# Performance work log

Measured on AMD Instinct MI355X. Metric: run time of the kernel, lower is better.

The kernel has to match this reference:

```python
import jax, jax.numpy as jnp
import numpy as np

B, T, F = 4096, 64, 32
U1, U2 = 256, 128  # stacked GRU: rnn_units, rnn_units // 2


def _gru_layer(x, Wg, bg, Wc, bc, units):
    """TF GRUCell semantics over a full sequence.
    x: [B, T, D]. Wg: [D+U, 2U], Wc: [D+U, U]. Returns outputs [B, T, U].
    r,u = sigmoid([x,h] Wg + bg); c = tanh([x, r*h] Wc + bc); h' = u*h + (1-u)*c
    """
    xT = jnp.swapaxes(x, 0, 1)  # [T, B, D]
    h0 = jnp.zeros((x.shape[0], units), x.dtype)

    def step(h, xt):
        gates = jax.nn.sigmoid(jnp.concatenate([xt, h], axis=-1) @ Wg + bg)
        r, u = jnp.split(gates, 2, axis=-1)
        c = jnp.tanh(jnp.concatenate([xt, r * h], axis=-1) @ Wc + bc)
        h_new = u * h + (1.0 - u) * c
        return h_new, h_new

    _, outs = jax.lax.scan(step, h0, xT)
    return jnp.swapaxes(outs, 0, 1)  # [B, T, U]


def setup_inputs() -> dict:
    key = jax.random.key(0)
    ks = jax.random.split(key, 12)
    s = 0.1
    inp = {
        "frames": jax.random.normal(ks[0], (B, T, F), jnp.float32),
        "W1_g": jax.random.normal(ks[1], (F + U1, 2 * U1), jnp.float32) * s,
        "b1_g": jnp.ones((2 * U1,), jnp.float32),  # TF gate bias init = 1.0
        "W1_c": jax.random.normal(ks[2], (F + U1, U1), jnp.float32) * s,
        "b1_c": jnp.zeros((U1,), jnp.float32),
        "W2_g": jax.random.normal(ks[3], (U1 + U2, 2 * U2), jnp.float32) * s,
        "b2_g": jnp.ones((2 * U2,), jnp.float32),
        "W2_c": jax.random.normal(ks[4], (U1 + U2, U2), jnp.float32) * s,
        "b2_c": jnp.zeros((U2,), jnp.float32),
        "Wd": jax.random.normal(ks[5], (U2, F), jnp.float32) * s,
        "bd": jnp.zeros((F,), jnp.float32),
    }
    return inp


def reference(frames, W1_g, b1_g, W1_c, b1_c, W2_g, b2_g, W2_c, b2_c, Wd, bd):
    # stacked GRU: MultiRNNCell([GRUCell(U1), GRUCell(U1 // 2)])
    h1 = _gru_layer(frames, W1_g, b1_g, W1_c, b1_c, U1)   # [B, T, U1]
    h2 = _gru_layer(h1, W2_g, b2_g, W2_c, b2_c, U2)       # [B, T, U2]
    last = h2[:, -1]                                       # use_cell_state=False -> outputs[:, -1]
    predicted = last @ Wd + bd                             # dense to sensor_count
    return predicted
```

## Files before the change

kernel.cpp:

```cpp
#include <hip/hip_runtime.h>


typedef unsigned short u16;
typedef __attribute__((ext_vector_type(8))) short bhalf8;
typedef __attribute__((ext_vector_type(4))) float fx4;

constexpr int Bc = 4096, Tc = 64, Fc = 32, U1 = 256, U2 = 128;
constexpr int K1 = Fc + U1;
constexpr int K2 = U1 + U2;
constexpr int NB = 16, NTHR = 512;
constexpr int LD1 = K1 + 8;
constexpr int LD2 = K2 + 8;

constexpr int nW1g = K1 * 512, nW1c = K1 * 256, nW2g = K2 * 256, nW2c = K2 * 128;
constexpr int oW1g = 0;
constexpr int oW1c = oW1g + nW1g;
constexpr int oW2g = oW1c + nW1c;
constexpr int oW2c = oW2g + nW2g;
constexpr int WTOT = oW2c + nW2c;
constexpr int nWdT = Fc * U2;

#define LGKM_BARRIER() asm volatile("s_waitcnt lgkmcnt(0)\n\ts_barrier" ::: "memory")

__device__ __forceinline__ u16 bf16_rne(float x) {
  unsigned u = __float_as_uint(x);
  return (u16)((u + 0x7fffu + ((u >> 16) & 1u)) >> 16);
}
__device__ __forceinline__ float bf16_f(u16 h) {
  return __uint_as_float(((unsigned)h) << 16);
}
__device__ __forceinline__ float sigm(float x) { return 1.0f / (1.0f + __expf(-x)); }
__device__ __forceinline__ float tanh_(float x) {
  x = fminf(fmaxf(x, -15.0f), 15.0f);
  const float s = __expf(2.0f * x);
  return (s - 1.0f) / (s + 1.0f);
}

__global__ void prep_weights(const float* __restrict__ W1g, const float* __restrict__ W1c,
                             const float* __restrict__ W2g, const float* __restrict__ W2c,
                             const float* __restrict__ Wd, u16* __restrict__ ws) {
  int j = blockIdx.x * 256 + threadIdx.x;
  if (j >= WTOT + nWdT) return;
  if (j >= WTOT) {
    const int jj = j - WTOT;
    float* wdT = (float*)(ws + WTOT);
    const int o = jj >> 7, c = jj & 127;
    wdT[jj] = Wd[c * Fc + o];
    return;
  }
  const float* src; u16* dst; int K, N, jj;
  if (j < nW1g)                    { src = W1g; K = K1; N = 512; jj = j;                      dst = ws + oW1g; }
  else if (j < nW1g + nW1c)        { src = W1c; K = K1; N = 256; jj = j - nW1g;               dst = ws + oW1c; }
  else if (j < nW1g + nW1c + nW2g) { src = W2g; K = K2; N = 256; jj = j - nW1g - nW1c;        dst = ws + oW2g; }
  else                             { src = W2c; K = K2; N = 128; jj = j - nW1g - nW1c - nW2g; dst = ws + oW2c; }
  int n = jj / K, k = jj - n * K;
  dst[(size_t)n * K + k] = bf16_rne(src[(size_t)k * N + n]);
}

template <int NT, int D>
struct Pipe {
  const u16* wp[NT];
  bhalf8 bb[D][NT];
  __device__ __forceinline__ void init(const u16* __restrict__ W, const int* n0,
                                       int K, int lc, int ao) {
#pragma unroll
    for (int i = 0; i < NT; ++i) wp[i] = W + (size_t)(n0[i] + lc) * K + ao;
  }
  __device__ __forceinline__ void prefetch() {
#pragma unroll
    for (int d = 0; d < D; ++d)
#pragma unroll
      for (int i = 0; i < NT; ++i) bb[d][i] = *(const bhalf8*)(wp[i] + d * 32);
  }
  template <int KT, int LDA>
  __device__ __forceinline__ void mm(fx4 (&acc)[NT], const u16 (&Ah)[16][LDA],
                                     const u16 (&Al)[16][LDA], int lc, int ao) {
#pragma unroll
    for (int kt = 0; kt < KT; ++kt) {
      const int k0 = kt * 32;
      const bhalf8 a_h = *(const bhalf8*)&Ah[lc][k0 + ao];
      const bhalf8 a_l = *(const bhalf8*)&Al[lc][k0 + ao];
#pragma unroll
      for (int i = 0; i < NT; ++i) {
        acc[i] = __builtin_amdgcn_mfma_f32_16x16x32_bf16(a_h, bb[kt % D][i], acc[i], 0, 0, 0);
        acc[i] = __builtin_amdgcn_mfma_f32_16x16x32_bf16(a_l, bb[kt % D][i], acc[i], 0, 0, 0);
      }
      if (kt + D < KT) {
#pragma unroll
        for (int i = 0; i < NT; ++i) bb[kt % D][i] = *(const bhalf8*)(wp[i] + (kt + D) * 32);
      }
    }
  }
};

__global__ __launch_bounds__(NTHR, 2)
void gru_mfma(const float* __restrict__ frames, const u16* __restrict__ ws,
              const float* __restrict__ b1g, const float* __restrict__ b1c,
              const float* __restrict__ b2g, const float* __restrict__ b2c,
              const float* __restrict__ bd, float* __restrict__ out) {
  __shared__ alignas(16) u16 A1h[16][LD1], A1l[16][LD1];
  __shared__ alignas(16) u16 A2h[16][LD2], A2l[16][LD2];

  const int tid = threadIdx.x;
  const int w = tid >> 6;
  const int l = tid & 63;
  const int lc = l & 15;
  const int lk = l >> 4;
  const int ao = lk * 8;
  const int row0 = lk * 4;
  const int b0 = blockIdx.x * NB;

  const float bg1r0 = b1g[w * 32 + lc],       bg1r1 = b1g[w * 32 + 16 + lc];
  const float bg1u0 = b1g[256 + w * 32 + lc], bg1u1 = b1g[256 + w * 32 + 16 + lc];
  const float bc10  = b1c[w * 32 + lc],       bc11  = b1c[w * 32 + 16 + lc];
  const float bg2r  = b2g[w * 16 + lc],       bg2u  = b2g[128 + w * 16 + lc];
  const float bc2v  = b2c[w * 16 + lc];

  Pipe<4, 4> pG1;  Pipe<2, 4> pC1;  Pipe<2, 4> pG2;  Pipe<1, 4> pC2;
  const int n0g1[4] = {w * 32, w * 32 + 16, 256 + w * 32, 256 + w * 32 + 16};
  const int n0c1[2] = {w * 32, w * 32 + 16};
  const int n0g2[2] = {w * 16, 128 + w * 16};
  const int n0c2[1] = {w * 16};
  pG1.init(ws + oW1g, n0g1, K1, lc, ao);
  pC1.init(ws + oW1c, n0c1, K1, lc, ao);
  pG2.init(ws + oW2g, n0g2, K2, lc, ao);
  pC2.init(ws + oW2c, n0c2, K2, lc, ao);

  for (int i = tid; i < 16 * LD1; i += NTHR) { (&A1h[0][0])[i] = 0; (&A1l[0][0])[i] = 0; }
  for (int i = tid; i < 16 * LD2; i += NTHR) { (&A2h[0][0])[i] = 0; (&A2l[0][0])[i] = 0; }

  const int xb = tid >> 5, xf = tid & 31;
  const float* fptr = frames + (size_t)(b0 + xb) * (Tc * Fc) + xf;

  {
    const float x0 = fptr[0];
    const u16 h = bf16_rne(x0);
    A1h[xb][xf] = h;
    A1l[xb][xf] = bf16_rne(x0 - bf16_f(h));
  }
  pG1.prefetch();
  LGKM_BARRIER();

  for (int t = 0; t < Tc; ++t) {
    const float xnxt = (t + 1 < Tc) ? fptr[(t + 1) * Fc] : 0.0f;

    fx4 acc[4] = { {bg1r0, bg1r0, bg1r0, bg1r0}, {bg1r1, bg1r1, bg1r1, bg1r1},
                   {bg1u0, bg1u0, bg1u0, bg1u0}, {bg1u1, bg1u1, bg1u1, bg1u1} };
    pG1.mm<9, LD1>(acc, A1h, A1l, lc, ao);
    pC1.prefetch();

    float hold1[2][4];
#pragma unroll
    for (int i = 0; i < 2; ++i)
#pragma unroll
      for (int q = 0; q < 4; ++q) {
        const int row = row0 + q, col = w * 32 + i * 16 + lc;
        hold1[i][q] = bf16_f(A1h[row][Fc + col]) + bf16_f(A1l[row][Fc + col]);
      }
    float rr[2][4], uu[2][4];
#pragma unroll
    for (int i = 0; i < 2; ++i)
#pragma unroll
      for (int q = 0; q < 4; ++q) { rr[i][q] = sigm(acc[i][q]); uu[i][q] = sigm(acc[2 + i][q]); }
    LGKM_BARRIER();

#pragma unroll
    for (int i = 0; i < 2; ++i)
#pragma unroll
      for (int q = 0; q < 4; ++q) {
        const int row = row0 + q, col = w * 32 + i * 16 + lc;
        const float rh = rr[i][q] * hold1[i][q];
        const u16 hh = bf16_rne(rh);
        A1h[row][Fc + col] = hh;
        A1l[row][Fc + col] = bf16_rne(rh - bf16_f(hh));
      }
    LGKM_BARRIER();

    fx4 accc[2] = { {bc10, bc10, bc10, bc10}, {bc11, bc11, bc11, bc11} };
    pC1.mm<9, LD1>(accc, A1h, A1l, lc, ao);
    pG2.prefetch();

    float hn1[2][4]; u16 hh1[2][4], hl1[2][4];
#pragma unroll
    for (int i = 0; i < 2; ++i)
#pragma unroll
      for (int q = 0; q < 4; ++q) {
        const float c = tanh_(accc[i][q]);
        const float hn = c + uu[i][q] * (hold1[i][q] - c);
        hh1[i][q] = bf16_rne(hn);
        hl1[i][q] = bf16_rne(hn - bf16_f(hh1[i][q]));
      }
    LGKM_BARRIER();
#pragma unroll
    for (int i = 0; i < 2; ++i)
#pragma unroll
      for (int q = 0; q < 4; ++q) {
        const int row = row0 + q, col = w * 32 + i * 16 + lc;
        A1h[row][Fc + col] = hh1[i][q];  A1l[row][Fc + col] = hl1[i][q];
        A2h[row][col] = hh1[i][q];       A2l[row][col] = hl1[i][q];
      }
    LGKM_BARRIER();

    fx4 acc2[2] = { {bg2r, bg2r, bg2r, bg2r}, {bg2u, bg2u, bg2u, bg2u} };
    pG2.mm<12, LD2>(acc2, A2h, A2l, lc, ao);
    pC2.prefetch();

    float hold2[4];
#pragma unroll
    for (int q = 0; q < 4; ++q) {
      const int row = row0 + q, col = w * 16 + lc;
      hold2[q] = bf16_f(A2h[row][U1 + col]) + bf16_f(A2l[row][U1 + col]);
    }
    float rr2[4], uu2[4];
#pragma unroll
    for (int q = 0; q < 4; ++q) { rr2[q] = sigm(acc2[0][q]); uu2[q] = sigm(acc2[1][q]); }
    LGKM_BARRIER();

#pragma unroll
    for (int q = 0; q < 4; ++q) {
      const int row = row0 + q, col = w * 16 + lc;
      const float rh = rr2[q] * hold2[q];
      const u16 hh = bf16_rne(rh);
      A2h[row][U1 + col] = hh;
      A2l[row][U1 + col] = bf16_rne(rh - bf16_f(hh));
    }
    LGKM_BARRIER();

    fx4 acc3[1] = { {bc2v, bc2v, bc2v, bc2v} };
    pC2.mm<12, LD2>(acc3, A2h, A2l, lc, ao);
    pG1.prefetch();
    LGKM_BARRIER();

#pragma unroll
    for (int q = 0; q < 4; ++q) {
      const int row = row0 + q, col = w * 16 + lc;
      const float c = tanh_(acc3[0][q]);
      const float hn = c + uu2[q] * (hold2[q] - c);
      const u16 hh = bf16_rne(hn);
      A2h[row][U1 + col] = hh;
      A2l[row][U1 + col] = bf16_rne(hn - bf16_f(hh));
    }
    {
      const u16 h = bf16_rne(xnxt);
      A1h[xb][xf] = h;
      A1l[xb][xf] = bf16_rne(xnxt - bf16_f(h));
    }
    LGKM_BARRIER();
  }

  {
    const float* wdT = (const float*)(ws + WTOT);
    const int o = tid & 31, b = tid >> 5;
    const float4* wrow = (const float4*)(wdT + o * 128);
    float acc = bd[o];
#pragma unroll 8
    for (int c4 = 0; c4 < 32; ++c4) {
      const float4 wv = wrow[c4];
      const int c = c4 * 4;
      const float h0 = bf16_f(A2h[b][U1 + c + 0]) + bf16_f(A2l[b][U1 + c + 0]);
      const float h1 = bf16_f(A2h[b][U1 + c + 1]) + bf16_f(A2l[b][U1 + c + 1]);
      const float h2 = bf16_f(A2h[b][U1 + c + 2]) + bf16_f(A2l[b][U1 + c + 2]);
      const float h3 = bf16_f(A2h[b][U1 + c + 3]) + bf16_f(A2l[b][U1 + c + 3]);
      acc = fmaf(h0, wv.x, fmaf(h1, wv.y, fmaf(h2, wv.z, fmaf(h3, wv.w, acc))));
    }
    out[(size_t)(b0 + b) * Fc + o] = acc;
  }
}

extern "C" void kernel_launch(void* const* d_in, const int* in_sizes, int n_in,
                              void* d_out, int out_size, void* d_ws, size_t ws_size,
                              hipStream_t stream) {
  const float* frames = (const float*)d_in[0];
  const float* W1g = (const float*)d_in[1];
  const float* b1g = (const float*)d_in[2];
  const float* W1c = (const float*)d_in[3];
  const float* b1c = (const float*)d_in[4];
  const float* W2g = (const float*)d_in[5];
  const float* b2g = (const float*)d_in[6];
  const float* W2c = (const float*)d_in[7];
  const float* b2c = (const float*)d_in[8];
  const float* Wd  = (const float*)d_in[9];
  const float* bd  = (const float*)d_in[10];
  u16* ws = (u16*)d_ws;
  float* outp = (float*)d_out;

  hipLaunchKernelGGL(prep_weights, dim3((WTOT + nWdT + 255) / 256), dim3(256), 0, stream,
                     W1g, W1c, W2g, W2c, Wd, ws);
  hipLaunchKernelGGL(gru_mfma, dim3(Bc / NB), dim3(NTHR), 0, stream,
                     frames, ws, b1g, b1c, b2g, b2c, bd, outp);
}
```

Measured before the change: 881.1 us.

## Write r*h into separate LDS buffers to drop per-step barriers

Stores r*h for both GRU layers in dedicated shared-memory buffers instead of overwriting the hidden state in place. This lets the kernel remove several block-wide barriers per timestep (from 7 to 4), since h_old no longer has to be protected before it is overwritten. It also merges the h_new compute and store loops and deepens the weight prefetch pipelines for three of the four matmuls (depth 4 raised to 6 or 8). The costs are more shared memory, now allocated dynamically, and more registers held by the deeper prefetch buffers, which could hurt occupancy at two blocks per CU.

```diff
diff --git a/kernel.cpp b/kernel.cpp
--- a/kernel.cpp
+++ b/kernel.cpp
@@ -2,6 +2,7 @@
 
 
 typedef unsigned short u16;
+typedef unsigned int u32;
 typedef __attribute__((ext_vector_type(8))) short bhalf8;
 typedef __attribute__((ext_vector_type(4))) float fx4;
 
@@ -9,8 +10,10 @@
 constexpr int K1 = Fc + U1;
 constexpr int K2 = U1 + U2;
 constexpr int NB = 16, NTHR = 512;
-constexpr int LD1 = K1 + 8;
-constexpr int LD2 = K2 + 8;
+constexpr int LD1 = 296;
+constexpr int LD2 = 392;
+constexpr int LDR1 = 264;
+constexpr int LDR2 = 136;
 
 constexpr int nW1g = K1 * 512, nW1c = K1 * 256, nW2g = K2 * 256, nW2c = K2 * 128;
 constexpr int oW1g = 0;
@@ -19,6 +22,17 @@
 constexpr int oW2c = oW2g + nW2g;
 constexpr int WTOT = oW2c + nW2c;
 constexpr int nWdT = Fc * U2;
+
+constexpr int oA1h = 0;
+constexpr int oA1l = oA1h + 16 * LD1;
+constexpr int oA2h = oA1l + 16 * LD1;
+constexpr int oA2l = oA2h + 16 * LD2;
+constexpr int oR1h = oA2l + 16 * LD2;
+constexpr int oR1l = oR1h + 16 * LDR1;
+constexpr int oR2h = oR1l + 16 * LDR1;
+constexpr int oR2l = oR2h + 16 * LDR2;
+constexpr int SM_TOT = oR2l + 16 * LDR2;
+constexpr size_t SMEM_BYTES = (size_t)SM_TOT * 2;
 
 #define LGKM_BARRIER() asm volatile("s_waitcnt lgkmcnt(0)\n\ts_barrier" ::: "memory")
 
@@ -57,7 +71,7 @@
   dst[(size_t)n * K + k] = bf16_rne(src[(size_t)k * N + n]);
 }
 
-template <int NT, int D>
+template <int NT, int D, int KT>
 struct Pipe {
   const u16* wp[NT];
   bhalf8 bb[D][NT];
@@ -72,34 +86,35 @@
 #pragma unroll
       for (int i = 0; i < NT; ++i) bb[d][i] = *(const bhalf8*)(wp[i] + d * 32);
   }
-  template <int KT, int LDA>
-  __device__ __forceinline__ void mm(fx4 (&acc)[NT], const u16 (&Ah)[16][LDA],
-                                     const u16 (&Al)[16][LDA], int lc, int ao) {
-#pragma unroll
-    for (int kt = 0; kt < KT; ++kt) {
-      const int k0 = kt * 32;
-      const bhalf8 a_h = *(const bhalf8*)&Ah[lc][k0 + ao];
-      const bhalf8 a_l = *(const bhalf8*)&Al[lc][k0 + ao];
-#pragma unroll
-      for (int i = 0; i < NT; ++i) {
-        acc[i] = __builtin_amdgcn_mfma_f32_16x16x32_bf16(a_h, bb[kt % D][i], acc[i], 0, 0, 0);
-        acc[i] = __builtin_amdgcn_mfma_f32_16x16x32_bf16(a_l, bb[kt % D][i], acc[i], 0, 0, 0);
-      }
-      if (kt + D < KT) {
-#pragma unroll
-        for (int i = 0; i < NT; ++i) bb[kt % D][i] = *(const bhalf8*)(wp[i] + (kt + D) * 32);
-      }
+  __device__ __forceinline__ void roll(int kt) {
+    if (kt + D < KT) {
+#pragma unroll
+      for (int i = 0; i < NT; ++i) bb[kt % D][i] = *(const bhalf8*)(wp[i] + (kt + D) * 32);
     }
   }
 };
+
+template <int NT, int D, int KT, typename P, typename LD>
+__device__ __forceinline__ void run_mm(P& p, fx4 (&acc)[NT], LD&& ld) {
+#pragma unroll
+  for (int kt = 0; kt < KT; ++kt) {
+    bhalf8 ah, al;
+    ld(kt, ah, al);
+#pragma unroll
+    for (int i = 0; i < NT; ++i) {
+      acc[i] = __builtin_amdgcn_mfma_f32_16x16x32_bf16(ah, p.bb[kt % D][i], acc[i], 0, 0, 0);
+      acc[i] = __builtin_amdgcn_mfma_f32_16x16x32_bf16(al, p.bb[kt % D][i], acc[i], 0, 0, 0);
+    }
+    p.roll(kt);
+  }
+}
 
 __global__ __launch_bounds__(NTHR, 2)
 void gru_mfma(const float* __restrict__ frames, const u16* __restrict__ ws,
               const float* __restrict__ b1g, const float* __restrict__ b1c,
               const float* __restrict__ b2g, const float* __restrict__ b2c,
               const float* __restrict__ bd, float* __restrict__ out) {
-  __shared__ alignas(16) u16 A1h[16][LD1], A1l[16][LD1];
-  __shared__ alignas(16) u16 A2h[16][LD2], A2l[16][LD2];
+  extern __shared__ u16 sm[];
 
   const int tid = threadIdx.x;
   const int w = tid >> 6;
@@ -116,7 +131,7 @@
   const float bg2r  = b2g[w * 16 + lc],       bg2u  = b2g[128 + w * 16 + lc];
   const float bc2v  = b2c[w * 16 + lc];
 
-  Pipe<4, 4> pG1;  Pipe<2, 4> pC1;  Pipe<2, 4> pG2;  Pipe<1, 4> pC2;
+  Pipe<4, 4, 9> pG1;  Pipe<2, 6, 9> pC1;  Pipe<2, 6, 12> pG2;  Pipe<1, 8, 12> pC2;
   const int n0g1[4] = {w * 32, w * 32 + 16, 256 + w * 32, 256 + w * 32 + 16};
   const int n0c1[2] = {w * 32, w * 32 + 16};
   const int n0g2[2] = {w * 16, 128 + w * 16};
@@ -126,8 +141,7 @@
   pG2.init(ws + oW2g, n0g2, K2, lc, ao);
   pC2.init(ws + oW2c, n0c2, K2, lc, ao);
 
-  for (int i = tid; i < 16 * LD1; i += NTHR) { (&A1h[0][0])[i] = 0; (&A1l[0][0])[i] = 0; }
-  for (int i = tid; i < 16 * LD2; i += NTHR) { (&A2h[0][0])[i] = 0; (&A2l[0][0])[i] = 0; }
+  for (int i = tid; i < SM_TOT; i += NTHR) sm[i] = 0;
 
   const int xb = tid >> 5, xf = tid & 31;
   const float* fptr = frames + (size_t)(b0 + xb) * (Tc * Fc) + xf;
@@ -135,101 +149,125 @@
   {
     const float x0 = fptr[0];
     const u16 h = bf16_rne(x0);
-    A1h[xb][xf] = h;
-    A1l[xb][xf] = bf16_rne(x0 - bf16_f(h));
+    sm[oA1h + xb * LD1 + xf] = h;
+    sm[oA1l + xb * LD1 + xf] = bf16_rne(x0 - bf16_f(h));
   }
   pG1.prefetch();
   LGKM_BARRIER();
 
+  auto ldG1 = [&](int kt, bhalf8& ah, bhalf8& al) {
+    const int idx = lc * LD1 + kt * 32 + ao;
+    ah = *(const bhalf8*)&sm[oA1h + idx];
+    al = *(const bhalf8*)&sm[oA1l + idx];
+  };
+  auto ldC1 = [&](int kt, bhalf8& ah, bhalf8& al) {
+    if (kt == 0) {
+      const int idx = lc * LD1 + ao;
+      ah = *(const bhalf8*)&sm[oA1h + idx];
+      al = *(const bhalf8*)&sm[oA1l + idx];
+    } else {
+      const int idx = lc * LDR1 + (kt - 1) * 32 + ao;
+      ah = *(const bhalf8*)&sm[oR1h + idx];
+      al = *(const bhalf8*)&sm[oR1l + idx];
+    }
+  };
+  auto ldG2 = [&](int kt, bhalf8& ah, bhalf8& al) {
+    const int idx = lc * LD2 + kt * 32 + ao;
+    ah = *(const bhalf8*)&sm[oA2h + idx];
+    al = *(const bhalf8*)&sm[oA2l + idx];
+  };
+  auto ldC2 = [&](int kt, bhalf8& ah, bhalf8& al) {
+    if (kt < 8) {
+      const int idx = lc * LD2 + kt * 32 + ao;
+      ah = *(const bhalf8*)&sm[oA2h + idx];
+      al = *(const bhalf8*)&sm[oA2l + idx];
+    } else {
+      const int idx = lc * LDR2 + (kt - 8) * 32 + ao;
+      ah = *(const bhalf8*)&sm[oR2h + idx];
+      al = *(const bhalf8*)&sm[oR2l + idx];
+    }
+  };
+
   for (int t = 0; t < Tc; ++t) {
-    const float xnxt = (t + 1 < Tc) ? fptr[(t + 1) * Fc] : 0.0f;
+    const float xn = (t + 1 < Tc) ? fptr[(t + 1) * Fc] : 0.0f;
 
     fx4 acc[4] = { {bg1r0, bg1r0, bg1r0, bg1r0}, {bg1r1, bg1r1, bg1r1, bg1r1},
                    {bg1u0, bg1u0, bg1u0, bg1u0}, {bg1u1, bg1u1, bg1u1, bg1u1} };
-    pG1.mm<9, LD1>(acc, A1h, A1l, lc, ao);
+    run_mm<4, 4, 9>(pG1, acc, ldG1);
     pC1.prefetch();
 
-    float hold1[2][4];
+    float hold1[2][4], uu[2][4];
 #pragma unroll
     for (int i = 0; i < 2; ++i)
 #pragma unroll
       for (int q = 0; q < 4; ++q) {
         const int row = row0 + q, col = w * 32 + i * 16 + lc;
-        hold1[i][q] = bf16_f(A1h[row][Fc + col]) + bf16_f(A1l[row][Fc + col]);
+        hold1[i][q] = bf16_f(sm[oA1h + row * LD1 + Fc + col]) +
+                      bf16_f(sm[oA1l + row * LD1 + Fc + col]);
+        uu[i][q] = sigm(acc[2 + i][q]);
       }
-    float rr[2][4], uu[2][4];
-#pragma unroll
-    for (int i = 0; i < 2; ++i)
-#pragma unroll
-      for (int q = 0; q < 4; ++q) { rr[i][q] = sigm(acc[i][q]); uu[i][q] = sigm(acc[2 + i][q]); }
-    LGKM_BARRIER();
-
 #pragma unroll
     for (int i = 0; i < 2; ++i)
 #pragma unroll
       for (int q = 0; q < 4; ++q) {
         const int row = row0 + q, col = w * 32 + i * 16 + lc;
-        const float rh = rr[i][q] * hold1[i][q];
+        const float rh = sigm(acc[i][q]) * hold1[i][q];
         const u16 hh = bf16_rne(rh);
-        A1h[row][Fc + col] = hh;
-        A1l[row][Fc + col] = bf16_rne(rh - bf16_f(hh));
+        sm[oR1h + row * LDR1 + col] = hh;
+        sm[oR1l + row * LDR1 + col] = bf16_rne(rh - bf16_f(hh));
       }
     LGKM_BARRIER();
 
     fx4 accc[2] = { {bc10, bc10, bc10, bc10}, {bc11, bc11, bc11, bc11} };
-    pC1.mm<9, LD1>(accc, A1h, A1l, lc, ao);
+    run_mm<2, 6, 9>(pC1, accc, ldC1);
     pG2.prefetch();
 
-    float hn1[2][4]; u16 hh1[2][4], hl1[2][4];
 #pragma unroll
     for (int i = 0; i < 2; ++i)
 #pragma unroll
       for (int q = 0; q < 4; ++q) {
+        const int row = row0 + q, col = w * 32 + i * 16 + lc;
         const float c = tanh_(accc[i][q]);
         const float hn = c + uu[i][q] * (hold1[i][q] - c);
-        hh1[i][q] = bf16_rne(hn);
-        hl1[i][q] = bf16_rne(hn - bf16_f(hh1[i][q]));
+        const u16 hh = bf16_rne(hn);
+        const u16 hl = bf16_rne(hn - bf16_f(hh));
+        sm[oA1h + row * LD1 + Fc + col] = hh;
+        sm[oA1l + row * LD1 + Fc + col] = hl;
+        sm[oA2h + row * LD2 + col] = hh;
+        sm[oA2l + row * LD2 + col] = hl;
       }
     LGKM_BARRIER();
-#pragma unroll
-    for (int i = 0; i < 2; ++i)
-#pragma unroll
-      for (int q = 0; q < 4; ++q) {
-        const int row = row0 + q, col = w * 32 + i * 16 + lc;
-        A1h[row][Fc + col] = hh1[i][q];  A1l[row][Fc + col] = hl1[i][q];
-        A2h[row][col] = hh1[i][q];       A2l[row][col] = hl1[i][q];
-      }
-    LGKM_BARRIER();
 
     fx4 acc2[2] = { {bg2r, bg2r, bg2r, bg2r}, {bg2u, bg2u, bg2u, bg2u} };
-    pG2.mm<12, LD2>(acc2, A2h, A2l, lc, ao);
+    run_mm<2, 6, 12>(pG2, acc2, ldG2);
     pC2.prefetch();
 
-    float hold2[4];
+    float hold2[4], uu2[4];
 #pragma unroll
     for (int q = 0; q < 4; ++q) {
       const int row = row0 + q, col = w * 16 + lc;
-      hold2[q] = bf16_f(A2h[row][U1 + col]) + bf16_f(A2l[row][U1 + col]);
-    }
-    float rr2[4], uu2[4];
-#pragma unroll
-    for (int q = 0; q < 4; ++q) { rr2[q] = sigm(acc2[0][q]); uu2[q] = sigm(acc2[1][q]); }
-    LGKM_BARRIER();
-
+      hold2[q] = bf16_f(sm[oA2h + row * LD2 + U1 + col]) +
+                 bf16_f(sm[oA2l + row * LD2 + U1 + col]);
+      uu2[q] = sigm(acc2[1][q]);
+    }
 #pragma unroll
     for (int q = 0; q < 4; ++q) {
       const int row = row0 + q, col = w * 16 + lc;
-      const float rh = rr2[q] * hold2[q];
+      const float rh = sigm(acc2[0][q]) * hold2[q];
       const u16 hh = bf16_rne(rh);
-      A2h[row][U1 + col] = hh;
-      A2l[row][U1 + col] = bf16_rne(rh - bf16_f(hh));
+      sm[oR2h + row * LDR2 + col] = hh;
+      sm[oR2l + row * LDR2 + col] = bf16_rne(rh - bf16_f(hh));
+    }
+    {
+      const u16 h = bf16_rne(xn);
+      sm[oA1h + xb * LD1 + xf] = h;
+      sm[oA1l + xb * LD1 + xf] = bf16_rne(xn - bf16_f(h));
     }
     LGKM_BARRIER();
 
     fx4 acc3[1] = { {bc2v, bc2v, bc2v, bc2v} };
-    pC2.mm<12, LD2>(acc3, A2h, A2l, lc, ao);
+    run_mm<1, 8, 12>(pC2, acc3, ldC2);
     pG1.prefetch();
-    LGKM_BARRIER();
 
 #pragma unroll
     for (int q = 0; q < 4; ++q) {
@@ -237,13 +275,8 @@
       const float c = tanh_(acc3[0][q]);
       const float hn = c + uu2[q] * (hold2[q] - c);
       const u16 hh = bf16_rne(hn);
-      A2h[row][U1 + col] = hh;
-      A2l[row][U1 + col] = bf16_rne(hn - bf16_f(hh));
-    }
-    {
-      const u16 h = bf16_rne(xnxt);
-      A1h[xb][xf] = h;
-      A1l[xb][xf] = bf16_rne(xnxt - bf16_f(h));
+      sm[oA2h + row * LD2 + U1 + col] = hh;
+      sm[oA2l + row * LD2 + U1 + col] = bf16_rne(hn - bf16_f(hh));
     }
     LGKM_BARRIER();
   }
@@ -257,10 +290,11 @@
     for (int c4 = 0; c4 < 32; ++c4) {
       const float4 wv = wrow[c4];
       const int c = c4 * 4;
-      const float h0 = bf16_f(A2h[b][U1 + c + 0]) + bf16_f(A2l[b][U1 + c + 0]);
-      const float h1 = bf16_f(A2h[b][U1 + c + 1]) + bf16_f(A2l[b][U1 + c + 1]);
-      const float h2 = bf16_f(A2h[b][U1 + c + 2]) + bf16_f(A2l[b][U1 + c + 2]);
-      const float h3 = bf16_f(A2h[b][U1 + c + 3]) + bf16_f(A2l[b][U1 + c + 3]);
+      const int base = b * LD2 + U1 + c;
+      const float h0 = bf16_f(sm[oA2h + base + 0]) + bf16_f(sm[oA2l + base + 0]);
+      const float h1 = bf16_f(sm[oA2h + base + 1]) + bf16_f(sm[oA2l + base + 1]);
+      const float h2 = bf16_f(sm[oA2h + base + 2]) + bf16_f(sm[oA2l + base + 2]);
+      const float h3 = bf16_f(sm[oA2h + base + 3]) + bf16_f(sm[oA2l + base + 3]);
       acc = fmaf(h0, wv.x, fmaf(h1, wv.y, fmaf(h2, wv.z, fmaf(h3, wv.w, acc))));
     }
     out[(size_t)(b0 + b) * Fc + o] = acc;
@@ -284,8 +318,11 @@
   u16* ws = (u16*)d_ws;
   float* outp = (float*)d_out;
 
+  hipFuncSetAttribute(reinterpret_cast<const void*>(gru_mfma),
+                      hipFuncAttributeMaxDynamicSharedMemorySize, (int)SMEM_BYTES);
+
   hipLaunchKernelGGL(prep_weights, dim3((WTOT + nWdT + 255) / 256), dim3(256), 0, stream,
                      W1g, W1c, W2g, W2c, Wd, ws);
-  hipLaunchKernelGGL(gru_mfma, dim3(Bc / NB), dim3(NTHR), 0, stream,
+  hipLaunchKernelGGL(gru_mfma, dim3(Bc / NB), dim3(NTHR), SMEM_BYTES, stream,
                      frames, ws, b1g, b1c, b2g, b2c, bd, outp);
 }
```

Measured after the change: 947.5 us. 7.5% more time.

## Skew the two GRU layers by one step and double-buffer hidden states

Applied to the files above, without the earlier changes.

Layer 2 now runs one timestep behind layer 1 inside the same loop iteration, with layer-1 hidden state and the input frame double-buffered in shared memory. Each iteration needs two barriers instead of six, and the gate and candidate matmuls of both layers are issued back to back, so the MFMA work in each phase is larger. The r*h operand is also stored only as a single bf16 value instead of a high/low pair, which halves those MFMAs but lowers precision on that term. The weight prefetch depth drops from 4 to 3 to offset the extra register pressure.

```diff
diff --git a/kernel.cpp b/kernel.cpp
--- a/kernel.cpp
+++ b/kernel.cpp
@@ -9,8 +9,9 @@
 constexpr int K1 = Fc + U1;
 constexpr int K2 = U1 + U2;
 constexpr int NB = 16, NTHR = 512;
-constexpr int LD1 = K1 + 8;
-constexpr int LD2 = K2 + 8;
+constexpr int LDX = 40;
+constexpr int LDH = 264;
+constexpr int LDH2 = 136;
 
 constexpr int nW1g = K1 * 512, nW1c = K1 * 256, nW2g = K2 * 256, nW2c = K2 * 128;
 constexpr int oW1g = 0;
@@ -19,6 +20,13 @@
 constexpr int oW2c = oW2g + nW2g;
 constexpr int WTOT = oW2c + nW2c;
 constexpr int nWdT = Fc * U2;
+
+constexpr int oXp  = 0;
+constexpr int oH1  = oXp + 4 * 16 * LDX;
+constexpr int oH2  = oH1 + 4 * 16 * LDH;
+constexpr int oRH1 = oH2 + 2 * 16 * LDH2;
+constexpr int oRH2 = oRH1 + 16 * LDH;
+constexpr int SM_TOT = oRH2 + 16 * LDH2;
 
 #define LGKM_BARRIER() asm volatile("s_waitcnt lgkmcnt(0)\n\ts_barrier" ::: "memory")
 
@@ -57,7 +65,7 @@
   dst[(size_t)n * K + k] = bf16_rne(src[(size_t)k * N + n]);
 }
 
-template <int NT, int D>
+template <int NT, int D, int KT>
 struct Pipe {
   const u16* wp[NT];
   bhalf8 bb[D][NT];
@@ -72,23 +80,10 @@
 #pragma unroll
       for (int i = 0; i < NT; ++i) bb[d][i] = *(const bhalf8*)(wp[i] + d * 32);
   }
-  template <int KT, int LDA>
-  __device__ __forceinline__ void mm(fx4 (&acc)[NT], const u16 (&Ah)[16][LDA],
-                                     const u16 (&Al)[16][LDA], int lc, int ao) {
-#pragma unroll
-    for (int kt = 0; kt < KT; ++kt) {
-      const int k0 = kt * 32;
-      const bhalf8 a_h = *(const bhalf8*)&Ah[lc][k0 + ao];
-      const bhalf8 a_l = *(const bhalf8*)&Al[lc][k0 + ao];
-#pragma unroll
-      for (int i = 0; i < NT; ++i) {
-        acc[i] = __builtin_amdgcn_mfma_f32_16x16x32_bf16(a_h, bb[kt % D][i], acc[i], 0, 0, 0);
-        acc[i] = __builtin_amdgcn_mfma_f32_16x16x32_bf16(a_l, bb[kt % D][i], acc[i], 0, 0, 0);
-      }
-      if (kt + D < KT) {
-#pragma unroll
-        for (int i = 0; i < NT; ++i) bb[kt % D][i] = *(const bhalf8*)(wp[i] + (kt + D) * 32);
-      }
+  __device__ __forceinline__ void roll(int kt) {
+    if (kt + D < KT) {
+#pragma unroll
+      for (int i = 0; i < NT; ++i) bb[kt % D][i] = *(const bhalf8*)(wp[i] + (kt + D) * 32);
     }
   }
 };
@@ -98,8 +93,7 @@
               const float* __restrict__ b1g, const float* __restrict__ b1c,
               const float* __restrict__ b2g, const float* __restrict__ b2c,
               const float* __restrict__ bd, float* __restrict__ out) {
-  __shared__ alignas(16) u16 A1h[16][LD1], A1l[16][LD1];
-  __shared__ alignas(16) u16 A2h[16][LD2], A2l[16][LD2];
+  __shared__ alignas(16) u16 sm[SM_TOT];
 
   const int tid = threadIdx.x;
   const int w = tid >> 6;
@@ -110,24 +104,24 @@
   const int row0 = lk * 4;
   const int b0 = blockIdx.x * NB;
 
-  const float bg1r0 = b1g[w * 32 + lc],       bg1r1 = b1g[w * 32 + 16 + lc];
-  const float bg1u0 = b1g[256 + w * 32 + lc], bg1u1 = b1g[256 + w * 32 + 16 + lc];
-  const float bc10  = b1c[w * 32 + lc],       bc11  = b1c[w * 32 + 16 + lc];
-  const float bg2r  = b2g[w * 16 + lc],       bg2u  = b2g[128 + w * 16 + lc];
-  const float bc2v  = b2c[w * 16 + lc];
-
-  Pipe<4, 4> pG1;  Pipe<2, 4> pC1;  Pipe<2, 4> pG2;  Pipe<1, 4> pC2;
+  const float bR0 = b1g[w * 32 + lc],       bR1 = b1g[w * 32 + 16 + lc];
+  const float bU0 = b1g[256 + w * 32 + lc], bU1 = b1g[256 + w * 32 + 16 + lc];
+  const float bC10 = b1c[w * 32 + lc],      bC11 = b1c[w * 32 + 16 + lc];
+  const float bR2 = b2g[w * 16 + lc];
+  const float bU2 = b2g[128 + w * 16 + lc];
+  const float bC2 = b2c[w * 16 + lc];
+
+  Pipe<4, 3, 9> pG1;  Pipe<2, 3, 12> pG2;  Pipe<2, 3, 9> pC1;  Pipe<1, 3, 12> pC2;
   const int n0g1[4] = {w * 32, w * 32 + 16, 256 + w * 32, 256 + w * 32 + 16};
+  const int n0g2[2] = {w * 16, 128 + w * 16};
   const int n0c1[2] = {w * 32, w * 32 + 16};
-  const int n0g2[2] = {w * 16, 128 + w * 16};
   const int n0c2[1] = {w * 16};
   pG1.init(ws + oW1g, n0g1, K1, lc, ao);
+  pG2.init(ws + oW2g, n0g2, K2, lc, ao);
   pC1.init(ws + oW1c, n0c1, K1, lc, ao);
-  pG2.init(ws + oW2g, n0g2, K2, lc, ao);
   pC2.init(ws + oW2c, n0c2, K2, lc, ao);
 
-  for (int i = tid; i < 16 * LD1; i += NTHR) { (&A1h[0][0])[i] = 0; (&A1l[0][0])[i] = 0; }
-  for (int i = tid; i < 16 * LD2; i += NTHR) { (&A2h[0][0])[i] = 0; (&A2l[0][0])[i] = 0; }
+  for (int i = tid; i < SM_TOT; i += NTHR) sm[i] = 0;
 
   const int xb = tid >> 5, xf = tid & 31;
   const float* fptr = frames + (size_t)(b0 + xb) * (Tc * Fc) + xf;
@@ -135,115 +129,168 @@
   {
     const float x0 = fptr[0];
     const u16 h = bf16_rne(x0);
-    A1h[xb][xf] = h;
-    A1l[xb][xf] = bf16_rne(x0 - bf16_f(h));
+    sm[oXp + xb * LDX + xf] = h;
+    sm[oXp + 16 * LDX + xb * LDX + xf] = bf16_rne(x0 - bf16_f(h));
   }
   pG1.prefetch();
+  pG2.prefetch();
   LGKM_BARRIER();
 
-  for (int t = 0; t < Tc; ++t) {
-    const float xnxt = (t + 1 < Tc) ? fptr[(t + 1) * Fc] : 0.0f;
-
-    fx4 acc[4] = { {bg1r0, bg1r0, bg1r0, bg1r0}, {bg1r1, bg1r1, bg1r1, bg1r1},
-                   {bg1u0, bg1u0, bg1u0, bg1u0}, {bg1u1, bg1u1, bg1u1, bg1u1} };
-    pG1.mm<9, LD1>(acc, A1h, A1l, lc, ao);
+  for (int s = 0; s <= Tc; ++s) {
+    const int cur = s & 1, prv = cur ^ 1;
+    const bool doL1 = (s < Tc), doL2 = (s > 0);
+    const int xpc = oXp + cur * (2 * 16 * LDX);
+    const int h1p = oH1 + prv * (2 * 16 * LDH);
+    const int h1c = oH1 + cur * (2 * 16 * LDH);
+    const float xn = (doL1 && s + 1 < Tc) ? fptr[(s + 1) * Fc] : 0.0f;
+
+    fx4 aG[4] = { {bR0, bR0, bR0, bR0}, {bR1, bR1, bR1, bR1},
+                  {bU0, bU0, bU0, bU0}, {bU1, bU1, bU1, bU1} };
+    if (doL1) {
+#pragma unroll
+      for (int kt = 0; kt < 9; ++kt) {
+        bhalf8 ah, al;
+        if (kt == 0) {
+          const int idx = lc * LDX + ao;
+          ah = *(const bhalf8*)&sm[xpc + idx];
+          al = *(const bhalf8*)&sm[xpc + 16 * LDX + idx];
+        } else {
+          const int idx = lc * LDH + (kt - 1) * 32 + ao;
+          ah = *(const bhalf8*)&sm[h1p + idx];
+          al = *(const bhalf8*)&sm[h1p + 16 * LDH + idx];
+        }
+#pragma unroll
+        for (int i = 0; i < 4; ++i) {
+          aG[i] = __builtin_amdgcn_mfma_f32_16x16x32_bf16(ah, pG1.bb[kt % 3][i], aG[i], 0, 0, 0);
+          aG[i] = __builtin_amdgcn_mfma_f32_16x16x32_bf16(al, pG1.bb[kt % 3][i], aG[i], 0, 0, 0);
+        }
+        pG1.roll(kt);
+      }
+    }
+    fx4 a2[2] = { {bR2, bR2, bR2, bR2}, {bU2, bU2, bU2, bU2} };
+    if (doL2) {
+#pragma unroll
+      for (int kt = 0; kt < 12; ++kt) {
+        bhalf8 ah, al;
+        if (kt < 8) {
+          const int idx = lc * LDH + kt * 32 + ao;
+          ah = *(const bhalf8*)&sm[h1p + idx];
+          al = *(const bhalf8*)&sm[h1p + 16 * LDH + idx];
+        } else {
+          const int idx = lc * LDH2 + (kt - 8) * 32 + ao;
+          ah = *(const bhalf8*)&sm[oH2 + idx];
+          al = *(const bhalf8*)&sm[oH2 + 16 * LDH2 + idx];
+        }
+#pragma unroll
+        for (int i = 0; i < 2; ++i) {
+          a2[i] = __builtin_amdgcn_mfma_f32_16x16x32_bf16(ah, pG2.bb[kt % 3][i], a2[i], 0, 0, 0);
+          a2[i] = __builtin_amdgcn_mfma_f32_16x16x32_bf16(al, pG2.bb[kt % 3][i], a2[i], 0, 0, 0);
+        }
+        pG2.roll(kt);
+      }
+    }
     pC1.prefetch();
-
-    float hold1[2][4];
-#pragma unroll
-    for (int i = 0; i < 2; ++i)
+    pC2.prefetch();
+
+    float hold1[2][4], uu1[2][4];
+    if (doL1) {
+#pragma unroll
+      for (int i = 0; i < 2; ++i)
+#pragma unroll
+        for (int q = 0; q < 4; ++q) {
+          const int row = row0 + q, col = w * 32 + i * 16 + lc;
+          hold1[i][q] = bf16_f(sm[h1p + row * LDH + col]) +
+                        bf16_f(sm[h1p + 16 * LDH + row * LDH + col]);
+          uu1[i][q] = sigm(aG[2 + i][q]);
+          sm[oRH1 + row * LDH + col] = bf16_rne(sigm(aG[i][q]) * hold1[i][q]);
+        }
+    }
+    float hold2[4], uu2[4];
+    if (doL2) {
 #pragma unroll
       for (int q = 0; q < 4; ++q) {
-        const int row = row0 + q, col = w * 32 + i * 16 + lc;
-        hold1[i][q] = bf16_f(A1h[row][Fc + col]) + bf16_f(A1l[row][Fc + col]);
-      }
-    float rr[2][4], uu[2][4];
-#pragma unroll
-    for (int i = 0; i < 2; ++i)
-#pragma unroll
-      for (int q = 0; q < 4; ++q) { rr[i][q] = sigm(acc[i][q]); uu[i][q] = sigm(acc[2 + i][q]); }
+        const int row = row0 + q, col = w * 16 + lc;
+        hold2[q] = bf16_f(sm[oH2 + row * LDH2 + col]) +
+                   bf16_f(sm[oH2 + 16 * LDH2 + row * LDH2 + col]);
+        uu2[q] = sigm(a2[1][q]);
+        sm[oRH2 + row * LDH2 + col] = bf16_rne(sigm(a2[0][q]) * hold2[q]);
+      }
+    }
     LGKM_BARRIER();
 
-#pragma unroll
-    for (int i = 0; i < 2; ++i)
+    fx4 aC1[2] = { {bC10, bC10, bC10, bC10}, {bC11, bC11, bC11, bC11} };
+    if (doL1) {
+#pragma unroll
+      for (int kt = 0; kt < 9; ++kt) {
+        if (kt == 0) {
+          const int idx = lc * LDX + ao;
+          const bhalf8 ah = *(const bhalf8*)&sm[xpc + idx];
+          const bhalf8 al = *(const bhalf8*)&sm[xpc + 16 * LDX + idx];
+#pragma unroll
+          for (int i = 0; i < 2; ++i) {
+            aC1[i] = __builtin_amdgcn_mfma_f32_16x16x32_bf16(ah, pC1.bb[0][i], aC1[i], 0, 0, 0);
+            aC1[i] = __builtin_amdgcn_mfma_f32_16x16x32_bf16(al, pC1.bb[0][i], aC1[i], 0, 0, 0);
+          }
+        } else {
+          const int idx = lc * LDH + (kt - 1) * 32 + ao;
+          const bhalf8 as = *(const bhalf8*)&sm[oRH1 + idx];
+#pragma unroll
+          for (int i = 0; i < 2; ++i)
+            aC1[i] = __builtin_amdgcn_mfma_f32_16x16x32_bf16(as, pC1.bb[kt % 3][i], aC1[i], 0, 0, 0);
+        }
+        pC1.roll(kt);
+      }
+    }
+    fx4 aC2 = {bC2, bC2, bC2, bC2};
+    if (doL2) {
+#pragma unroll
+      for (int kt = 0; kt < 12; ++kt) {
+        if (kt < 8) {
+          const int idx = lc * LDH + kt * 32 + ao;
+          const bhalf8 ah = *(const bhalf8*)&sm[h1p + idx];
+          const bhalf8 al = *(const bhalf8*)&sm[h1p + 16 * LDH + idx];
+          aC2 = __builtin_amdgcn_mfma_f32_16x16x32_bf16(ah, pC2.bb[kt % 3][0], aC2, 0, 0, 0);
+          aC2 = __builtin_amdgcn_mfma_f32_16x16x32_bf16(al, pC2.bb[kt % 3][0], aC2, 0, 0, 0);
+        } else {
+          const int idx = lc * LDH2 + (kt - 8) * 32 + ao;
+          const bhalf8 as = *(const bhalf8*)&sm[oRH2 + idx];
+          aC2 = __builtin_amdgcn_mfma_f32_16x16x32_bf16(as, pC2.bb[kt % 3][0], aC2, 0, 0, 0);
+        }
+        pC2.roll(kt);
+      }
+    }
+    pG1.prefetch();
+    pG2.prefetch();
+
+    if (doL1) {
+#pragma unroll
+      for (int i = 0; i < 2; ++i)
+#pragma unroll
+        for (int q = 0; q < 4; ++q) {
+          const int row = row0 + q, col = w * 32 + i * 16 + lc;
+          const float c = tanh_(aC1[i][q]);
+          const float hn = c + uu1[i][q] * (hold1[i][q] - c);
+          const u16 hh = bf16_rne(hn);
+          sm[h1c + row * LDH + col] = hh;
+          sm[h1c + 16 * LDH + row * LDH + col] = bf16_rne(hn - bf16_f(hh));
+        }
+    }
+    if (doL2) {
 #pragma unroll
       for (int q = 0; q < 4; ++q) {
-        const int row = row0 + q, col = w * 32 + i * 16 + lc;
-        const float rh = rr[i][q] * hold1[i][q];
-        const u16 hh = bf16_rne(rh);
-        A1h[row][Fc + col] = hh;
-        A1l[row][Fc + col] = bf16_rne(rh - bf16_f(hh));
-      }
-    LGKM_BARRIER();
-
-    fx4 accc[2] = { {bc10, bc10, bc10, bc10}, {bc11, bc11, bc11, bc11} };
-    pC1.mm<9, LD1>(accc, A1h, A1l, lc, ao);
-    pG2.prefetch();
-
-    float hn1[2][4]; u16 hh1[2][4], hl1[2][4];
-#pragma unroll
-    for (int i = 0; i < 2; ++i)
-#pragma unroll
-      for (int q = 0; q < 4; ++q) {
-        const float c = tanh_(accc[i][q]);
-        const float hn = c + uu[i][q] * (hold1[i][q] - c);
-        hh1[i][q] = bf16_rne(hn);
-        hl1[i][q] = bf16_rne(hn - bf16_f(hh1[i][q]));
-      }
-    LGKM_BARRIER();
-#pragma unroll
-    for (int i = 0; i < 2; ++i)
-#pragma unroll
-      for (int q = 0; q < 4; ++q) {
-        const int row = row0 + q, col = w * 32 + i * 16 + lc;
-        A1h[row][Fc + col] = hh1[i][q];  A1l[row][Fc + col] = hl1[i][q];
-        A2h[row][col] = hh1[i][q];       A2l[row][col] = hl1[i][q];
-      }
-    LGKM_BARRIER();
-
-    fx4 acc2[2] = { {bg2r, bg2r, bg2r, bg2r}, {bg2u, bg2u, bg2u, bg2u} };
-    pG2.mm<12, LD2>(acc2, A2h, A2l, lc, ao);
-    pC2.prefetch();
-
-    float hold2[4];
-#pragma unroll
-    for (int q = 0; q < 4; ++q) {
-      const int row = row0 + q, col = w * 16 + lc;
-      hold2[q] = bf16_f(A2h[row][U1 + col]) + bf16_f(A2l[row][U1 + col]);
-    }
-    float rr2[4], uu2[4];
-#pragma unroll
-    for (int q = 0; q < 4; ++q) { rr2[q] = sigm(acc2[0][q]); uu2[q] = sigm(acc2[1][q]); }
-    LGKM_BARRIER();
-
-#pragma unroll
-    for (int q = 0; q < 4; ++q) {
-      const int row = row0 + q, col = w * 16 + lc;
-      const float rh = rr2[q] * hold2[q];
-      const u16 hh = bf16_rne(rh);
-      A2h[row][U1 + col] = hh;
-      A2l[row][U1 + col] = bf16_rne(rh - bf16_f(hh));
-    }
-    LGKM_BARRIER();
-
-    fx4 acc3[1] = { {bc2v, bc2v, bc2v, bc2v} };
-    pC2.mm<12, LD2>(acc3, A2h, A2l, lc, ao);
-    pG1.prefetch();
-    LGKM_BARRIER();
-
-#pragma unroll
-    for (int q = 0; q < 4; ++q) {
-      const int row = row0 + q, col = w * 16 + lc;
-      const float c = tanh_(acc3[0][q]);
-      const float hn = c + uu2[q] * (hold2[q] - c);
-      const u16 hh = bf16_rne(hn);
-      A2h[row][U1 + col] = hh;
-      A2l[row][U1 + col] = bf16_rne(hn - bf16_f(hh));
-    }
-    {
-      const u16 h = bf16_rne(xnxt);
-      A1h[xb][xf] = h;
-      A1l[xb][xf] = bf16_rne(xnxt - bf16_f(h));
+        const int row = row0 + q, col = w * 16 + lc;
+        const float c = tanh_(aC2[q]);
+        const float hn = c + uu2[q] * (hold2[q] - c);
+        const u16 hh = bf16_rne(hn);
+        sm[oH2 + row * LDH2 + col] = hh;
+        sm[oH2 + 16 * LDH2 + row * LDH2 + col] = bf16_rne(hn - bf16_f(hh));
+      }
+    }
+    if (doL1 && s + 1 < Tc) {
+      const int xpn = oXp + ((s + 1) & 1) * (2 * 16 * LDX);
+      const u16 h = bf16_rne(xn);
+      sm[xpn + xb * LDX + xf] = h;
+      sm[xpn + 16 * LDX + xb * LDX + xf] = bf16_rne(xn - bf16_f(h));
     }
     LGKM_BARRIER();
   }
@@ -257,10 +304,11 @@
     for (int c4 = 0; c4 < 32; ++c4) {
       const float4 wv = wrow[c4];
       const int c = c4 * 4;
-      const float h0 = bf16_f(A2h[b][U1 + c + 0]) + bf16_f(A2l[b][U1 + c + 0]);
-      const float h1 = bf16_f(A2h[b][U1 + c + 1]) + bf16_f(A2l[b][U1 + c + 1]);
-      const float h2 = bf16_f(A2h[b][U1 + c + 2]) + bf16_f(A2l[b][U1 + c + 2]);
-      const float h3 = bf16_f(A2h[b][U1 + c + 3]) + bf16_f(A2l[b][U1 + c + 3]);
+      const int base = b * LDH2 + c;
+      const float h0 = bf16_f(sm[oH2 + base + 0]) + bf16_f(sm[oH2 + 16 * LDH2 + base + 0]);
+      const float h1 = bf16_f(sm[oH2 + base + 1]) + bf16_f(sm[oH2 + 16 * LDH2 + base + 1]);
+      const float h2 = bf16_f(sm[oH2 + base + 2]) + bf16_f(sm[oH2 + 16 * LDH2 + base + 2]);
+      const float h3 = bf16_f(sm[oH2 + base + 3]) + bf16_f(sm[oH2 + 16 * LDH2 + base + 3]);
       acc = fmaf(h0, wv.x, fmaf(h1, wv.y, fmaf(h2, wv.z, fmaf(h3, wv.w, acc))));
     }
     out[(size_t)(b0 + b) * Fc + o] = acc;
```

After: 979.8 us. +11.2%, slower.
